# Kernel tuning notes

Hardware: AMD Instinct MI355X
Metric: run time of the kernel (lower is better)

## Reference

```python
import jax, jax.numpy as jnp
import numpy as np

THRESHOLD = 0.95


def setup_inputs() -> dict:
    key = jax.random.key(0)
    k1, k2 = jax.random.split(key, 2)
    B, T, D = 16, 2048, 1024
    hs = jax.random.normal(k1, (B, T, D), dtype=jnp.float32)
    hs_mask = jnp.ones((B, 1, T), dtype=jnp.float32)
    w = jax.random.normal(k2, (D,), dtype=jnp.float32) * 0.02  # project.weight [1,D] -> [D]
    b = jnp.zeros((), dtype=jnp.float32)                        # project.bias
    return {"hs": hs, "hs_mask": hs_mask, "w": w, "b": b}


def reference(hs, hs_mask, w, b):
    B, T, D = hs.shape
    # project + sigmoid + mask
    x = jnp.einsum("btd,d->bt", hs, w) + b            # [B,T]
    alphas_s = jax.nn.sigmoid(x)
    alphas = alphas_s * hs_mask[:, 0, :]              # [B,T]

    # ---- integrate-and-fire scan over time ----
    def step(carry, inp):
        integrate, frame = carry                      # [B], [B,D]
        alpha, h = inp                                # [B], [B,D]
        dist_completion = 1.0 - integrate
        integrate = integrate + alpha
        fire_val = integrate                          # recorded pre-reset value
        fireplace = integrate > THRESHOLD
        integrate = jnp.where(fireplace, integrate - 1.0, integrate)
        cur = jnp.where(fireplace, dist_completion, alpha)
        frame_out = frame + cur[:, None] * h          # recorded frame at t
        frame_next = jnp.where(fireplace[:, None], (alpha - cur)[:, None] * h, frame_out)
        return (integrate, frame_next), (fire_val, frame_out)

    init = (jnp.zeros((B,), hs.dtype), jnp.zeros((B, D), hs.dtype))
    _, (fires_t, frames_t) = jax.lax.scan(
        step, init, (jnp.swapaxes(alphas, 0, 1), jnp.swapaxes(hs, 0, 1)))
    fires = jnp.swapaxes(fires_t, 0, 1)               # [B,T]
    frames = jnp.swapaxes(frames_t, 0, 1)             # [B,T,D]

    # ---- gather fired frames, left-packed, padded to static L=T ----
    fired = fires > THRESHOLD                         # [B,T]
    pos = jnp.cumsum(fired.astype(jnp.int32), axis=1) - 1
    L = T                                             # static upper bound on label length
    pos = jnp.where(fired, pos, L)                    # out-of-range -> dropped
    bidx = jnp.broadcast_to(jnp.arange(B, dtype=jnp.int32)[:, None], (B, T))
    out = jnp.zeros((B, L, D), hs.dtype).at[bidx, pos].set(frames, mode="drop")

    len_labels = jnp.round(alphas.sum(-1)).astype(jnp.int32)          # [B]
    new_masks = (jnp.arange(L)[None, :] < len_labels[:, None])[:, None, :]  # [B,1,L] bool
    return out, new_masks
```

## Files before the change

### kernel.cpp

```cpp
#include <hip/hip_runtime.h>
#include <math.h>

#define BB 16
#define TT 2048
#define DD 1024
#define THRESH 0.95f
#define RPB 8

typedef float nt4 __attribute__((ext_vector_type(4)));

__device__ __forceinline__ void nt_store4(const float4& v, float4* p) {
    nt4 x = {v.x, v.y, v.z, v.w};
    __builtin_nontemporal_store(x, (nt4*)p);
}

__global__ __launch_bounds__(256) void proj_kernel(
    const float* __restrict__ hs, const float* __restrict__ hs_mask,
    const float* __restrict__ w, const float* __restrict__ bias,
    float* __restrict__ alphas)
{
    int row  = blockIdx.x * 4 + (threadIdx.x >> 6);
    int lane = threadIdx.x & 63;
    const float4* hp = (const float4*)(hs + (size_t)row * DD);
    const float4* wp = (const float4*)w;
    float sum = 0.f;
#pragma unroll
    for (int j = 0; j < 4; ++j) {
        float4 h4 = hp[lane + 64 * j];
        float4 w4 = wp[lane + 64 * j];
        sum += h4.x * w4.x + h4.y * w4.y + h4.z * w4.z + h4.w * w4.w;
    }
#pragma unroll
    for (int off = 32; off; off >>= 1) sum += __shfl_down(sum, off, 64);
    if (lane == 0) {
        float x  = sum + bias[0];
        float al = 1.f / (1.f + expf(-x));
        alphas[row] = al * hs_mask[row];
    }
}


#define SCAN_GROUP(RREG, GIDX)                                                \
    {                                                                         \
        float cv = 0.f, pv = 0.f;                                             \
        _Pragma("unroll 16")                                                  \
        for (int j = 0; j < 64; ++j) {                                        \
            float a = __int_as_float(                                         \
                __builtin_amdgcn_readlane(__float_as_int(RREG), j));          \
            float pre  = integ + a;                         \
            bool  fire = pre > THRESH;                      \
            float c    = fire ? dist : a;                                     \
            integ      = fire ? pre - 1.f : pre;        \
            dist       = 1.f - integ;                                         \
            bool sel   = (lane == j);                                         \
            cv = sel ? c   : cv;                                              \
            pv = sel ? pre : pv;                                              \
        }                                                                     \
        cp[(GIDX) * 64 + lane] = cv;                                          \
        unsigned long long bm = __ballot(pv > THRESH);                        \
        gmask = (lane == (GIDX)) ? bm : gmask;                                \
    }

__global__ __launch_bounds__(64) void scan_kernel(
    const float* __restrict__ alphas, float* __restrict__ cur,
    int* __restrict__ fire_times, int* __restrict__ n_fires,
    int* __restrict__ len_labels, float* __restrict__ out_mask)
{
    int b    = blockIdx.x;
    int lane = threadIdx.x;
    const float* ap = alphas + (size_t)b * TT;
    float*       cp = cur    + (size_t)b * TT;

    unsigned long long gmask = 0ull;
    float integ = 0.f, dist = 1.f;
    double dsum = 0.0;

    for (int outer = 0; outer < 4; ++outer) {
        int base = outer * 512 + lane;
        float r0 = ap[base +   0];
        float r1 = ap[base +  64];
        float r2 = ap[base + 128];
        float r3 = ap[base + 192];
        float r4 = ap[base + 256];
        float r5 = ap[base + 320];
        float r6 = ap[base + 384];
        float r7 = ap[base + 448];
        dsum += (double)r0 + (double)r1 + (double)r2 + (double)r3
              + (double)r4 + (double)r5 + (double)r6 + (double)r7;
        int gb = outer * 8;
        SCAN_GROUP(r0, gb + 0)
        SCAN_GROUP(r1, gb + 1)
        SCAN_GROUP(r2, gb + 2)
        SCAN_GROUP(r3, gb + 3)
        SCAN_GROUP(r4, gb + 4)
        SCAN_GROUP(r5, gb + 5)
        SCAN_GROUP(r6, gb + 6)
        SCAN_GROUP(r7, gb + 7)
    }

#pragma unroll
    for (int off = 32; off; off >>= 1) dsum += __shfl_down(dsum, off, 64);
    int len = __double2int_rn(dsum);
    len = __shfl(len, 0, 64);
    if (lane == 0) len_labels[b] = len;

    float* mp = out_mask + (size_t)b * TT;
#pragma unroll
    for (int j = 0; j < TT / 64; ++j)
        mp[j * 64 + lane] = ((j * 64 + lane) < len) ? 1.f : 0.f;

    int cnt  = __popcll(gmask);
    int pref = cnt;
#pragma unroll
    for (int off = 1; off < 64; off <<= 1) {
        int y = __shfl_up(pref, off, 64);
        if (lane >= off) pref += y;
    }
    int pos = pref - cnt;
    unsigned long long m = gmask;
    int baset = lane * 64;
    int* fp = fire_times + (size_t)b * TT;
    while (m) {
        int j = __ffsll(m) - 1;
        fp[pos++] = baset + j;
        m &= m - 1;
    }
    if (lane == 63) n_fires[b] = pref;
}

__global__ __launch_bounds__(256) void gather_kernel(
    const float* __restrict__ hs, const float* __restrict__ alphas,
    const float* __restrict__ cur, const int* __restrict__ fire_times,
    const int* __restrict__ n_fires, float* __restrict__ out)
{
    int chunk = blockIdx.x;
    int b  = chunk >> 8;
    int r0 = (chunk & 255) * RPB;
    int ti = threadIdx.x;
    int nf = n_fires[b];

    float4* ob = (float4*)(out + ((size_t)b * TT + r0) * DD);

    if (r0 >= nf) {
        float4 z = {0.f, 0.f, 0.f, 0.f};
#pragma unroll
        for (int i = 0; i < RPB; ++i)
            nt_store4(z, &ob[i * 256 + ti]);
        return;
    }

    const int*    ft  = fire_times + (size_t)b * TT;
    const float*  al  = alphas     + (size_t)b * TT;
    const float*  cu  = cur        + (size_t)b * TT;
    const float4* hsb = (const float4*)(hs + (size_t)b * TT * DD);

    int    t;
    float4 hprev = {0.f, 0.f, 0.f, 0.f};
    float  wprev = 0.f;
    bool   have_prev;
    if (r0 == 0) {
        t = 0;
        have_prev = false;
    } else {
        int tp = ft[r0 - 1];
        t = tp + 1;
        hprev = hsb[(size_t)tp * 256 + ti];
        wprev = al[tp] - cu[tp];
        have_prev = true;
    }

#pragma unroll
    for (int i = 0; i < RPB; ++i) {
        int r = r0 + i;
        float4 a = {0.f, 0.f, 0.f, 0.f};
        if (r < nf) {
            if (have_prev) {
                a.x = wprev * hprev.x; a.y = wprev * hprev.y;
                a.z = wprev * hprev.z; a.w = wprev * hprev.w;
            }
            int te = ft[r];
            for (;;) {
                float4 h  = hsb[(size_t)t * 256 + ti];
                float  cw = cu[t];
                a.x += cw * h.x; a.y += cw * h.y;
                a.z += cw * h.z; a.w += cw * h.w;
                if (t == te) {
                    wprev = al[t] - cw;
                    hprev = h;
                    ++t;
                    break;
                }
                ++t;
            }
            have_prev = true;
        }
        nt_store4(a, &ob[i * 256 + ti]);
    }
}

extern "C" void kernel_launch(void* const* d_in, const int* in_sizes, int n_in,
                              void* d_out, int out_size, void* d_ws, size_t ws_size,
                              hipStream_t stream) {
    const float* hs      = (const float*)d_in[0];
    const float* hs_mask = (const float*)d_in[1];
    const float* w       = (const float*)d_in[2];
    const float* bias    = (const float*)d_in[3];

    float* out      = (float*)d_out;
    float* out_mask = out + (size_t)BB * TT * DD;

    float* alphas     = (float*)d_ws;
    float* cur        = alphas + BB * TT;
    int*   fire_times = (int*)(cur + BB * TT);
    int*   n_fires    = fire_times + BB * TT;
    int*   len_labels = n_fires + BB;

    proj_kernel<<<BB * TT / 4, 256, 0, stream>>>(hs, hs_mask, w, bias, alphas);
    scan_kernel<<<BB, 64, 0, stream>>>(alphas, cur, fire_times, n_fires,
                                       len_labels, out_mask);
    gather_kernel<<<BB * (TT / RPB), 256, 0, stream>>>(hs, alphas, cur, fire_times,
                                                       n_fires, out);
}
```

Measured before the change: 302.8 us.

## Fuse projection, scan and gather into one cooperative persistent kernel

Replaces the three launches with a single cooperative kernel. All blocks first compute the projection and sigmoid, then meet at a grid sync. Afterwards 16 blocks run the per-batch scans and publish fire counts per 512-step pass through release-atomic progress counters, while the remaining blocks gather frames as soon as enough fires are available. The aim is to cut launch gaps and overlap the serial scan with the bandwidth-bound gather. The cost is spin-waiting, a grid barrier, and a requirement that 1024 blocks be co-resident. If the cooperative launch fails, it falls back to the old three-kernel path.

```diff
diff --git a/kernel.cpp b/kernel.cpp
--- a/kernel.cpp
+++ b/kernel.cpp
@@ -1,11 +1,18 @@
 #include <hip/hip_runtime.h>
+#include <hip/hip_cooperative_groups.h>
 #include <math.h>
+
+namespace cg = cooperative_groups;
 
 #define BB 16
 #define TT 2048
 #define DD 1024
 #define THRESH 0.95f
 #define RPB 8
+#define NCHUNK (BB * (TT / RPB))
+#define NBLK 1024
+#define GBLK (NBLK - BB)
+#define DONEBIT 0x40000000u
 
 typedef float nt4 __attribute__((ext_vector_type(4)));
 
@@ -13,32 +20,6 @@
     nt4 x = {v.x, v.y, v.z, v.w};
     __builtin_nontemporal_store(x, (nt4*)p);
 }
-
-__global__ __launch_bounds__(256) void proj_kernel(
-    const float* __restrict__ hs, const float* __restrict__ hs_mask,
-    const float* __restrict__ w, const float* __restrict__ bias,
-    float* __restrict__ alphas)
-{
-    int row  = blockIdx.x * 4 + (threadIdx.x >> 6);
-    int lane = threadIdx.x & 63;
-    const float4* hp = (const float4*)(hs + (size_t)row * DD);
-    const float4* wp = (const float4*)w;
-    float sum = 0.f;
-#pragma unroll
-    for (int j = 0; j < 4; ++j) {
-        float4 h4 = hp[lane + 64 * j];
-        float4 w4 = wp[lane + 64 * j];
-        sum += h4.x * w4.x + h4.y * w4.y + h4.z * w4.z + h4.w * w4.w;
-    }
-#pragma unroll
-    for (int off = 32; off; off >>= 1) sum += __shfl_down(sum, off, 64);
-    if (lane == 0) {
-        float x  = sum + bias[0];
-        float al = 1.f / (1.f + expf(-x));
-        alphas[row] = al * hs_mask[row];
-    }
-}
-
 
 #define SCAN_GROUP(RREG, GIDX)                                                \
     {                                                                         \
@@ -61,10 +42,230 @@
         gmask = (lane == (GIDX)) ? bm : gmask;                                \
     }
 
+__global__ __launch_bounds__(256, 4) void fused_kernel(
+    const float* __restrict__ hs, const float* __restrict__ hs_mask,
+    const float* __restrict__ w, const float* __restrict__ bias,
+    float* __restrict__ out, float* __restrict__ out_mask,
+    float* __restrict__ alphas, float* __restrict__ cur,
+    int* __restrict__ fire_times, unsigned* __restrict__ progress)
+{
+    __shared__ int s_nf;
+
+    {
+        int lane = threadIdx.x & 63;
+        const float4* wp = (const float4*)w;
+        float4 w0 = wp[lane], w1 = wp[lane + 64],
+               w2 = wp[lane + 128], w3 = wp[lane + 192];
+        int row0 = blockIdx.x * (BB * TT / NBLK) + (threadIdx.x >> 6);
+#pragma unroll
+        for (int it = 0; it < (BB * TT / NBLK); it += 4) {
+            int row = row0 + it;
+            const float4* hp = (const float4*)(hs + (size_t)row * DD);
+            float4 h0 = hp[lane], h1 = hp[lane + 64],
+                   h2 = hp[lane + 128], h3 = hp[lane + 192];
+            float sum = h0.x * w0.x + h0.y * w0.y + h0.z * w0.z + h0.w * w0.w
+                      + h1.x * w1.x + h1.y * w1.y + h1.z * w1.z + h1.w * w1.w
+                      + h2.x * w2.x + h2.y * w2.y + h2.z * w2.z + h2.w * w2.w
+                      + h3.x * w3.x + h3.y * w3.y + h3.z * w3.z + h3.w * w3.w;
+#pragma unroll
+            for (int off = 32; off; off >>= 1) sum += __shfl_down(sum, off, 64);
+            if (lane == 0) {
+                float x  = sum + bias[0];
+                float al = 1.f / (1.f + expf(-x));
+                alphas[row] = al * hs_mask[row];
+            }
+        }
+        if (blockIdx.x == 0 && threadIdx.x < BB) progress[threadIdx.x] = 0u;
+    }
+
+    cg::this_grid().sync();
+
+    if (blockIdx.x < BB) {
+        if (threadIdx.x >= 64) return;
+        int b    = blockIdx.x;
+        int lane = threadIdx.x;
+        const float* ap = alphas + (size_t)b * TT;
+        float*       cp = cur    + (size_t)b * TT;
+        int*         fp = fire_times + (size_t)b * TT;
+
+        unsigned long long gmask = 0ull;
+        float integ = 0.f, dist = 1.f;
+        double dsum = 0.0;
+        int base_fires = 0;
+
+        for (int outer = 0; outer < 4; ++outer) {
+            int base = outer * 512 + lane;
+            float r0 = ap[base +   0];
+            float r1 = ap[base +  64];
+            float r2 = ap[base + 128];
+            float r3 = ap[base + 192];
+            float r4 = ap[base + 256];
+            float r5 = ap[base + 320];
+            float r6 = ap[base + 384];
+            float r7 = ap[base + 448];
+            dsum += (double)r0 + (double)r1 + (double)r2 + (double)r3
+                  + (double)r4 + (double)r5 + (double)r6 + (double)r7;
+            int gb = outer * 8;
+            SCAN_GROUP(r0, gb + 0)
+            SCAN_GROUP(r1, gb + 1)
+            SCAN_GROUP(r2, gb + 2)
+            SCAN_GROUP(r3, gb + 3)
+            SCAN_GROUP(r4, gb + 4)
+            SCAN_GROUP(r5, gb + 5)
+            SCAN_GROUP(r6, gb + 6)
+            SCAN_GROUP(r7, gb + 7)
+
+            bool inpass = (lane >= gb) && (lane < gb + 8);
+            unsigned long long mym = inpass ? gmask : 0ull;
+            int cnt  = __popcll(mym);
+            int pref = cnt;
+#pragma unroll
+            for (int off = 1; off < 64; off <<= 1) {
+                int y = __shfl_up(pref, off, 64);
+                if (lane >= off) pref += y;
+            }
+            int pass_total = __shfl(pref, 63, 64);
+            int pos = base_fires + pref - cnt;
+            unsigned long long m = mym;
+            int baset = lane * 64;
+            while (m) {
+                int j = __ffsll(m) - 1;
+                fp[pos++] = baset + j;
+                m &= m - 1;
+            }
+            base_fires += pass_total;
+
+            __threadfence();
+            if (lane == 0) {
+                unsigned val = (outer == 3) ? ((unsigned)base_fires | DONEBIT)
+                                            : (unsigned)base_fires;
+                __hip_atomic_store(&progress[b], val, __ATOMIC_RELEASE,
+                                   __HIP_MEMORY_SCOPE_AGENT);
+            }
+        }
+
+#pragma unroll
+        for (int off = 32; off; off >>= 1) dsum += __shfl_down(dsum, off, 64);
+        int len = __double2int_rn(dsum);
+        len = __shfl(len, 0, 64);
+        float* mp = out_mask + (size_t)b * TT;
+#pragma unroll
+        for (int j = 0; j < TT / 64; ++j)
+            mp[j * 64 + lane] = ((j * 64 + lane) < len) ? 1.f : 0.f;
+        return;
+    }
+
+    int gk = blockIdx.x - BB;
+    int ti = threadIdx.x;
+    for (int c = gk; c < NCHUNK; c += GBLK) {
+        int b  = c & (BB - 1);
+        int r0 = (c >> 4) * RPB;
+
+        if (threadIdx.x == 0) {
+            int need = r0 + RPB;
+            unsigned v;
+            for (;;) {
+                v = __hip_atomic_load(&progress[b], __ATOMIC_ACQUIRE,
+                                      __HIP_MEMORY_SCOPE_AGENT);
+                if (v & DONEBIT) { v &= ~DONEBIT; break; }
+                if ((int)v >= need) break;
+                __builtin_amdgcn_s_sleep(2);
+            }
+            s_nf = (int)v;
+        }
+        __syncthreads();
+        int nf = s_nf;
+        __syncthreads();
+
+        float4* ob = (float4*)(out + ((size_t)b * TT + r0) * DD);
+
+        if (r0 >= nf) {
+            float4 z = {0.f, 0.f, 0.f, 0.f};
+#pragma unroll
+            for (int i = 0; i < RPB; ++i)
+                nt_store4(z, &ob[i * 256 + ti]);
+            continue;
+        }
+
+        const int*    ft  = fire_times + (size_t)b * TT;
+        const float*  al  = alphas     + (size_t)b * TT;
+        const float*  cu  = cur        + (size_t)b * TT;
+        const float4* hsb = (const float4*)(hs + (size_t)b * TT * DD);
+
+        int    t;
+        float4 hprev = {0.f, 0.f, 0.f, 0.f};
+        float  wprev = 0.f;
+        bool   have_prev;
+        if (r0 == 0) {
+            t = 0;
+            have_prev = false;
+        } else {
+            int tp = ft[r0 - 1];
+            t = tp + 1;
+            hprev = hsb[(size_t)tp * 256 + ti];
+            wprev = al[tp] - cu[tp];
+            have_prev = true;
+        }
+
+#pragma unroll
+        for (int i = 0; i < RPB; ++i) {
+            int r = r0 + i;
+            float4 a = {0.f, 0.f, 0.f, 0.f};
+            if (r < nf) {
+                if (have_prev) {
+                    a.x = wprev * hprev.x; a.y = wprev * hprev.y;
+                    a.z = wprev * hprev.z; a.w = wprev * hprev.w;
+                }
+                int te = ft[r];
+                for (;;) {
+                    float4 h  = hsb[(size_t)t * 256 + ti];
+                    float  cw = cu[t];
+                    a.x += cw * h.x; a.y += cw * h.y;
+                    a.z += cw * h.z; a.w += cw * h.w;
+                    if (t == te) {
+                        wprev = al[t] - cw;
+                        hprev = h;
+                        ++t;
+                        break;
+                    }
+                    ++t;
+                }
+                have_prev = true;
+            }
+            nt_store4(a, &ob[i * 256 + ti]);
+        }
+    }
+}
+
+__global__ __launch_bounds__(256) void proj_kernel(
+    const float* __restrict__ hs, const float* __restrict__ hs_mask,
+    const float* __restrict__ w, const float* __restrict__ bias,
+    float* __restrict__ alphas)
+{
+    int row  = blockIdx.x * 4 + (threadIdx.x >> 6);
+    int lane = threadIdx.x & 63;
+    const float4* hp = (const float4*)(hs + (size_t)row * DD);
+    const float4* wp = (const float4*)w;
+    float sum = 0.f;
+#pragma unroll
+    for (int j = 0; j < 4; ++j) {
+        float4 h4 = hp[lane + 64 * j];
+        float4 w4 = wp[lane + 64 * j];
+        sum += h4.x * w4.x + h4.y * w4.y + h4.z * w4.z + h4.w * w4.w;
+    }
+#pragma unroll
+    for (int off = 32; off; off >>= 1) sum += __shfl_down(sum, off, 64);
+    if (lane == 0) {
+        float x  = sum + bias[0];
+        float al = 1.f / (1.f + expf(-x));
+        alphas[row] = al * hs_mask[row];
+    }
+}
+
 __global__ __launch_bounds__(64) void scan_kernel(
     const float* __restrict__ alphas, float* __restrict__ cur,
     int* __restrict__ fire_times, int* __restrict__ n_fires,
-    int* __restrict__ len_labels, float* __restrict__ out_mask)
+    float* __restrict__ out_mask)
 {
     int b    = blockIdx.x;
     int lane = threadIdx.x;
@@ -102,7 +303,6 @@
     for (int off = 32; off; off >>= 1) dsum += __shfl_down(dsum, off, 64);
     int len = __double2int_rn(dsum);
     len = __shfl(len, 0, 64);
-    if (lane == 0) len_labels[b] = len;
 
     float* mp = out_mask + (size_t)b * TT;
 #pragma unroll
@@ -209,15 +409,23 @@
     float* out      = (float*)d_out;
     float* out_mask = out + (size_t)BB * TT * DD;
 
-    float* alphas     = (float*)d_ws;
-    float* cur        = alphas + BB * TT;
-    int*   fire_times = (int*)(cur + BB * TT);
-    int*   n_fires    = fire_times + BB * TT;
-    int*   len_labels = n_fires + BB;
-
-    proj_kernel<<<BB * TT / 4, 256, 0, stream>>>(hs, hs_mask, w, bias, alphas);
-    scan_kernel<<<BB, 64, 0, stream>>>(alphas, cur, fire_times, n_fires,
-                                       len_labels, out_mask);
-    gather_kernel<<<BB * (TT / RPB), 256, 0, stream>>>(hs, alphas, cur, fire_times,
-                                                       n_fires, out);
-}
+    float*    alphas     = (float*)d_ws;
+    float*    cur        = alphas + BB * TT;
+    int*      fire_times = (int*)(cur + BB * TT);
+    int*      n_fires    = fire_times + BB * TT;
+    unsigned* progress   = (unsigned*)(n_fires + BB);
+
+    void* args[] = {(void*)&hs, (void*)&hs_mask, (void*)&w, (void*)&bias,
+                    (void*)&out, (void*)&out_mask, (void*)&alphas, (void*)&cur,
+                    (void*)&fire_times, (void*)&progress};
+    hipError_t e = hipLaunchCooperativeKernel((const void*)fused_kernel,
+                                              dim3(NBLK), dim3(256),
+                                              args, 0, stream);
+    if (e != hipSuccess) {
+        proj_kernel<<<BB * TT / 4, 256, 0, stream>>>(hs, hs_mask, w, bias, alphas);
+        scan_kernel<<<BB, 64, 0, stream>>>(alphas, cur, fire_times, n_fires,
+                                           out_mask);
+        gather_kernel<<<BB * (TT / RPB), 256, 0, stream>>>(hs, alphas, cur,
+                                                           fire_times, n_fires, out);
+    }
+}
```

Result: slower. 476.9 us (+57.5%).
